# Kernel optimization log

Hardware: AMD Instinct MI355X
Metric: run time of the kernel (lower is better)

Reference implementation:

```python
import jax, jax.numpy as jnp
import numpy as np

B, S, D, H = 64, 128, 1024, 512
N = 2 * S - 1          # total tree nodes (leaves + internal)
NSTEP = S - 1          # number of binary compositions
NW, NP = 511, 152      # word / phrase category counts


def _l2n(x):
    return x / jnp.clip(jnp.linalg.norm(x, axis=-1, keepdims=True), 1e-12)


def circular_correlation(a, b):
    a, b = _l2n(a), _l2n(b)
    c = jnp.fft.irfft(jnp.conj(jnp.fft.rfft(a)) * jnp.fft.rfft(b), n=H)
    return _l2n(c)


def _lstm_dir(x, w_ih, w_hh, b):
    # x: [B,S,D] -> hs: [B,S,H]; PyTorch gate order i,f,g,o
    xp = jnp.einsum('bsd,gd->bsg', x, w_ih) + b  # precompute input proj

    def step(carry, xt):
        h, c = carry
        g = xt + h @ w_hh.T
        i, f, gg, o = jnp.split(g, 4, axis=-1)
        c = jax.nn.sigmoid(f) * c + jax.nn.sigmoid(i) * jnp.tanh(gg)
        h = jax.nn.sigmoid(o) * jnp.tanh(c)
        return (h, c), h

    h0 = jnp.zeros((x.shape[0], H), x.dtype)
    _, hs = jax.lax.scan(step, (h0, h0), xp.transpose(1, 0, 2))
    return hs.transpose(1, 0, 2)


def setup_inputs():
    key = jax.random.key(0)
    ks = jax.random.split(key, 12)
    sc = 0.05
    elmo_rep = jax.random.normal(ks[0], (B, S, D), jnp.float32)
    w_ih_f = jax.random.normal(ks[1], (4 * H, D), jnp.float32) * sc
    w_hh_f = jax.random.normal(ks[2], (4 * H, H), jnp.float32) * sc
    b_f = jnp.zeros((4 * H,), jnp.float32)
    w_ih_b = jax.random.normal(ks[3], (4 * H, D), jnp.float32) * sc
    w_hh_b = jax.random.normal(ks[4], (4 * H, H), jnp.float32) * sc
    b_b = jnp.zeros((4 * H,), jnp.float32)
    W1 = jax.random.normal(ks[5], (H, H), jnp.float32) * sc
    W2 = jax.random.normal(ks[6], (H, H), jnp.float32) * sc
    word_W = jax.random.normal(ks[7], (NW, H), jnp.float32) * sc
    word_b = jnp.zeros((NW,), jnp.float32)
    phrase_W = jax.random.normal(ks[8], (NP, H), jnp.float32) * sc
    phrase_b = jnp.zeros((NP,), jnp.float32)
    # valid binary-tree composition schedule: parent S+i, children < S+i
    rng = np.random.default_rng(0)
    comp = np.zeros((B, NSTEP, 4), np.int32)
    comp[:, :, 0] = 2
    for i in range(NSTEP):
        comp[:, i, 1] = S + i
        comp[:, i, 2] = rng.integers(0, S + i, size=B)
        comp[:, i, 3] = rng.integers(0, S + i, size=B)
    composition_info = jnp.asarray(comp)
    pos = jnp.stack([jnp.arange(S), jnp.arange(S)], axis=1).astype(jnp.int32)
    original_pos = jnp.tile(pos[None], (B, 1, 1))
    batch_label = jax.random.randint(ks[9], (B, N), 0, NW, dtype=jnp.int64)
    return dict(elmo_rep=elmo_rep, w_ih_f=w_ih_f, w_hh_f=w_hh_f, b_f=b_f,
                w_ih_b=w_ih_b, w_hh_b=w_hh_b, b_b=b_b, W1=W1, W2=W2,
                word_W=word_W, word_b=word_b, phrase_W=phrase_W,
                phrase_b=phrase_b, composition_info=composition_info,
                original_pos=original_pos, batch_label=batch_label)


def reference(elmo_rep, w_ih_f, w_hh_f, b_f, w_ih_b, w_hh_b, b_b, W1, W2,
              word_W, word_b, phrase_W, phrase_b, composition_info,
              original_pos, batch_label):
    # BiLSTM over ELMo reps (all sequences full length S)
    fwd = _lstm_dir(elmo_rep, w_ih_f, w_hh_f, b_f)
    bwd = _lstm_dir(elmo_rep[:, ::-1], w_ih_b, w_hh_b, b_b)[:, ::-1]
    combined = jax.nn.leaky_relu(fwd @ W1.T + bwd @ W2.T, negative_slope=0.01)

    # scatter leaves into node buffer [B,N,H], then L2-normalize
    bidx = jnp.arange(B)[:, None]
    tgt = original_pos[:, :, 0]
    src = original_pos[:, :, 1]
    vector = jnp.zeros((B, N, H), combined.dtype)
    vector = vector.at[bidx, tgt].set(combined[bidx, src])
    vector = _l2n(vector)

    # sequential per-depth compose: gather children, circular-correlate, scatter parent
    b = jnp.arange(B)

    def step(vec, info):  # info: [B,4] = [type, parent, left, right]
        t, p, l, r = info[:, 0], info[:, 1], info[:, 2], info[:, 3]
        lv = vec[b, l]
        rv = vec[b, r]
        comp = circular_correlation(lv, rv)
        cur = vec[b, p]
        val = jnp.where((t == 1)[:, None], lv,
                        jnp.where((t == 2)[:, None], comp, cur))
        return vec.at[b, p].set(val), None

    vector, _ = jax.lax.scan(step, vector, composition_info.transpose(1, 0, 2))

    # words = leaf nodes (first S slots), phrases = internal nodes
    word_vector = vector[:, :S].reshape(-1, H)
    phrase_vector = vector[:, S:].reshape(-1, H)
    word_label = batch_label[:, :S].reshape(-1)
    phrase_label = batch_label[:, S:].reshape(-1)
    word_output = word_vector @ word_W.T + word_b
    phrase_output = phrase_vector @ phrase_W.T + phrase_b
    return word_output, phrase_output, word_label, phrase_label
```

## Files before the change

kernel.cpp:

```cpp
#include <hip/hip_runtime.h>
#include <math.h>

#define NB 64
#define NS 128
#define ND 1024
#define NH 512
#define NG 2048
#define NTOT 255
#define NSTEPS 127
#define NWV 511
#define NPV 152

static const size_t XPB_SZ = (size_t)2 * NS * NG * NB;
static const size_t H_SZ   = (size_t)2 * NS * NH * NB;
static const size_t VEC_SZ = (size_t)NB * NTOT * NH;
static const size_t HB_SZ  = (size_t)2 * NS * NH * NB;
static const size_t EB_SZ  = (size_t)NB * NS * ND;
static const size_t WB_SZ  = (size_t)4096 * ND;
static const size_t W12_SZ = (size_t)2 * NH * NH;
static const size_t WO_SZ  = (size_t)512 * NH;
static const size_t VB_SZ  = (size_t)NB * NS * NH;
static const size_t VP_SZ  = (size_t)8192 * NH;
static const size_t WP_SZ  = (size_t)256 * NH;
#define BAR_TOT (127 * 2 * 32 * 32)

typedef __attribute__((ext_vector_type(8))) short short8v;
typedef __attribute__((ext_vector_type(8))) unsigned short ushort8v;
typedef __attribute__((ext_vector_type(4))) float float4v;

__device__ __forceinline__ float sigm(float x) { return 1.f / (1.f + __expf(-x)); }
__device__ __forceinline__ float tanh_fast(float x) {
  const float e = __expf(2.f * x);
  return 1.f - 2.f / (e + 1.f);
}
__device__ __forceinline__ unsigned short f2bf(float x) {
  unsigned b = __float_as_uint(x);
  return (unsigned short)((b + 0x7FFFu + ((b >> 16) & 1u)) >> 16);
}
__device__ __forceinline__ float bf2f(unsigned short u) {
  return __uint_as_float(((unsigned)u) << 16);
}

__global__ __launch_bounds__(256) void k_cvt(
    const float* __restrict__ elmo, const float* __restrict__ wf,
    const float* __restrict__ wb, const float* __restrict__ W1,
    const float* __restrict__ W2, const float* __restrict__ wordW,
    const float* __restrict__ phraseW,
    unsigned short* __restrict__ elmo_bf, unsigned short* __restrict__ W_bf,
    unsigned short* __restrict__ W12_bf, unsigned short* __restrict__ wout_bf,
    unsigned short* __restrict__ wp_bf, int* __restrict__ bar) {
  const int gid = blockIdx.x * 256 + threadIdx.x;
  if (gid < BAR_TOT) bar[gid] = 0;
  const int NE4 = (NB * NS * ND) / 4;
  const int NW4 = (4096 * ND) / 4;
  const int NW4h = NW4 / 2;
  const int N12 = (int)(W12_SZ / 4);
  const int NWO = (int)(WO_SZ / 4);
  const int NWO_real = (NWV * NH) / 4;
  const int NP4 = (int)(WP_SZ / 4);
  const int NP4_real = (NPV * NH) / 4;
  const int TOT = NE4 + NW4 + N12 + NWO + NP4;
  for (int i = gid; i < TOT; i += gridDim.x * 256) {
    float4 v = make_float4(0.f, 0.f, 0.f, 0.f);
    unsigned short* dst;
    if (i < NE4) {
      const int e0 = i << 2;
      const int b = e0 >> 17;
      const int t = (e0 >> 10) & 127;
      const int k = e0 & 1023;
      v = *(const float4*)(elmo + e0);
      dst = elmo_bf + ((size_t)((t << 6) + b) << 10) + k;
    } else if (i < NE4 + NW4) {
      const int j = i - NE4;
      v = (j < NW4h) ? *(const float4*)(wf + ((size_t)j << 2))
                     : *(const float4*)(wb + ((size_t)(j - NW4h) << 2));
      dst = W_bf + ((size_t)j << 2);
    } else if (i < NE4 + NW4 + N12) {
      const int j = i - NE4 - NW4;
      const int half = N12 / 2;
      v = (j < half) ? *(const float4*)(W1 + ((size_t)j << 2))
                     : *(const float4*)(W2 + ((size_t)(j - half) << 2));
      dst = W12_bf + ((size_t)j << 2);
    } else if (i < NE4 + NW4 + N12 + NWO) {
      const int j = i - NE4 - NW4 - N12;
      if (j < NWO_real) v = *(const float4*)(wordW + ((size_t)j << 2));
      dst = wout_bf + ((size_t)j << 2);
    } else {
      const int j = i - NE4 - NW4 - N12 - NWO;
      if (j < NP4_real) v = *(const float4*)(phraseW + ((size_t)j << 2));
      dst = wp_bf + ((size_t)j << 2);
    }
    uint2 u;
    u.x = (unsigned)f2bf(v.x) | ((unsigned)f2bf(v.y) << 16);
    u.y = (unsigned)f2bf(v.z) | ((unsigned)f2bf(v.w) << 16);
    *(uint2*)dst = u;
  }
}

__global__ __launch_bounds__(256) void k_xp(
    const unsigned short* __restrict__ elmo_bf,
    const unsigned short* __restrict__ W_bf,
    const float* __restrict__ biasf, const float* __restrict__ biasb,
    unsigned short* __restrict__ xpb) {
  __shared__ unsigned short As[128 * 64];
  __shared__ unsigned short Bs[128 * 64];
  const int tid = threadIdx.x;
  const int n0 = blockIdx.x * 128;
  const int m0 = blockIdx.y * 128;
  const int wv = tid >> 6, lane = tid & 63;
  const int cl = lane & 15, bq = lane >> 4;
  const int wm = (wv >> 1) << 6;
  const int wn = (wv & 1) << 6;
  const int sr = tid >> 1, skc = (tid & 1) << 5;
  const unsigned short* asrc = elmo_bf + (size_t)(m0 + sr) * ND + skc;
  const unsigned short* bsrc = W_bf + (size_t)(n0 + sr) * ND + skc;
  const int sswz = (sr & 15) << 3;
  float4v acc[4][4];
#pragma unroll
  for (int nt = 0; nt < 4; ++nt) {
    const int n = n0 + wn + nt * 16 + cl;
    const float bv = (n < 2048) ? biasf[n] : biasb[n - 2048];
#pragma unroll
    for (int mt = 0; mt < 4; ++mt) acc[mt][nt] = (float4v){bv, bv, bv, bv};
  }
  for (int k0 = 0; k0 < ND; k0 += 64) {
    ushort8v av4[4], bv4[4];
#pragma unroll
    for (int i = 0; i < 4; ++i) av4[i] = *(const ushort8v*)(asrc + k0 + 8 * i);
#pragma unroll
    for (int i = 0; i < 4; ++i) bv4[i] = *(const ushort8v*)(bsrc + k0 + 8 * i);
    __syncthreads();
#pragma unroll
    for (int i = 0; i < 4; ++i) {
      *(ushort8v*)&As[((sr << 6) + skc + 8 * i) ^ sswz] = av4[i];
      *(ushort8v*)&Bs[((sr << 6) + skc + 8 * i) ^ sswz] = bv4[i];
    }
    __syncthreads();
#pragma unroll
    for (int ks = 0; ks < 2; ++ks) {
      const int koff = (ks << 5) + (bq << 3);
      short8v af[4], bf_[4];
#pragma unroll
      for (int mt = 0; mt < 4; ++mt) {
        const int ar = wm + mt * 16 + cl;
        af[mt] = *(const short8v*)&As[((ar << 6) + koff) ^ ((ar & 15) << 3)];
      }
#pragma unroll
      for (int nt = 0; nt < 4; ++nt) {
        const int br = wn + nt * 16 + cl;
        bf_[nt] = *(const short8v*)&Bs[((br << 6) + koff) ^ ((br & 15) << 3)];
      }
#pragma unroll
      for (int mt = 0; mt < 4; ++mt)
#pragma unroll
        for (int nt = 0; nt < 4; ++nt)
          acc[mt][nt] =
              __builtin_amdgcn_mfma_f32_16x16x32_bf16(af[mt], bf_[nt], acc[mt][nt], 0, 0, 0);
    }
  }
#pragma unroll
  for (int mt = 0; mt < 4; ++mt) {
    const int mbase = m0 + wm + mt * 16 + (bq << 2);
    const int t = mbase >> 6, b4 = mbase & 63;
#pragma unroll
    for (int nt = 0; nt < 4; ++nt) {
      const int n = n0 + wn + nt * 16 + cl;
      const int dir = n >> 11, grow = n & 2047;
      const int g = grow >> 9, cb = (grow & 511) >> 4;
      const float4v a = acc[mt][nt];
      uint2 u;
      u.x = (unsigned)f2bf(a[0]) | ((unsigned)f2bf(a[1]) << 16);
      u.y = (unsigned)f2bf(a[2]) | ((unsigned)f2bf(a[3]) << 16);
      const size_t idx =
          ((((size_t)(dir * NS + t) * 32 + cb) * 4 + g) << 10) + (cl << 6) + b4;
      *(uint2*)&xpb[idx] = u;
    }
  }
}

__global__ __launch_bounds__(256) void k_lstm(
    const float* __restrict__ whh_f, const float* __restrict__ whh_b,
    const unsigned short* __restrict__ xpb,
    unsigned short* __restrict__ h_bf, int* __restrict__ bar) {
  __shared__ unsigned short WS[64 * 512];
  __shared__ unsigned short hOut[64 * 16];
  const int bid = blockIdx.x;
  const int dir = bid >> 5;
  const int cb = bid & 31;
  const int col0 = cb << 4;
  const int tid = threadIdx.x;
  const int lane = tid & 63;
  const int w = tid >> 6;
  const int cl = lane & 15, bq = lane >> 4;
  const int b4 = (w << 4) + (bq << 2);
  const int arow = (w << 4) + cl;
  const float* whh = dir ? whh_b : whh_f;

  {
    const int gr = tid >> 2;
    const int kc = (tid & 3) << 7;
    const int gg = gr >> 4, cc = gr & 15;
    const float* src = whh + (size_t)(gg * NH + col0 + cc) * NH + kc;
    const int swz = (gr & 15) << 3;
#pragma unroll
    for (int i = 0; i < 16; ++i) {
      const float4 f0 = *(const float4*)(src + 8 * i);
      const float4 f1 = *(const float4*)(src + 8 * i + 4);
      ushort8v u;
      u[0] = f2bf(f0.x); u[1] = f2bf(f0.y); u[2] = f2bf(f0.z); u[3] = f2bf(f0.w);
      u[4] = f2bf(f1.x); u[5] = f2bf(f1.y); u[6] = f2bf(f1.z); u[7] = f2bf(f1.w);
      *(ushort8v*)&WS[((gr << 9) + kc + 8 * i) ^ swz] = u;
    }
  }
  __syncthreads();

  unsigned short* hb_us = h_bf + ((size_t)dir * NS << 15);
  unsigned long long* hb_ull = (unsigned long long*)h_bf + ((size_t)dir * NS << 12);

  float4v c4 = {0.f, 0.f, 0.f, 0.f};

  uint2 xg0, xg1, xg2, xg3, xn0, xn1, xn2, xn3;
  {
    const int p0 = dir ? (NS - 1) : 0;
    const unsigned short* xc = xpb + (((size_t)(dir * NS + p0) * 32 + cb) << 12);
    xg0 = *(const uint2*)&xc[(0 << 10) + (cl << 6) + b4];
    xg1 = *(const uint2*)&xc[(1 << 10) + (cl << 6) + b4];
    xg2 = *(const uint2*)&xc[(2 << 10) + (cl << 6) + b4];
    xg3 = *(const uint2*)&xc[(3 << 10) + (cl << 6) + b4];
    const int p1 = dir ? (NS - 2) : 1;
    const unsigned short* xc1 = xpb + (((size_t)(dir * NS + p1) * 32 + cb) << 12);
    xn0 = *(const uint2*)&xc1[(0 << 10) + (cl << 6) + b4];
    xn1 = *(const uint2*)&xc1[(1 << 10) + (cl << 6) + b4];
    xn2 = *(const uint2*)&xc1[(2 << 10) + (cl << 6) + b4];
    xn3 = *(const uint2*)&xc1[(3 << 10) + (cl << 6) + b4];
  }

  for (int t = 0; t < NS; ++t) {
    const int pos = dir ? (NS - 1 - t) : t;
    const int t2 = (t + 2 < NS) ? (t + 2) : (NS - 1);
    const int p2 = dir ? (NS - 1 - t2) : t2;
    const unsigned short* xc2 =
        xpb + (((size_t)(dir * NS + p2) * 32 + cb) << 12);
    const uint2 pf0 = *(const uint2*)&xc2[(0 << 10) + (cl << 6) + b4];
    const uint2 pf1 = *(const uint2*)&xc2[(1 << 10) + (cl << 6) + b4];
    const uint2 pf2 = *(const uint2*)&xc2[(2 << 10) + (cl << 6) + b4];
    const uint2 pf3 = *(const uint2*)&xc2[(3 << 10) + (cl << 6) + b4];

    float4v acc[4] = {{0.f, 0.f, 0.f, 0.f}, {0.f, 0.f, 0.f, 0.f},
                      {0.f, 0.f, 0.f, 0.f}, {0.f, 0.f, 0.f, 0.f}};
    if (t > 0) {
      const int prevpos = dir ? (pos + 1) : (pos - 1);
      const unsigned long long* hsrc = hb_ull + ((size_t)prevpos << 13);
      unsigned long long ha0[16], ha1[16];
#pragma unroll
      for (int ks = 0; ks < 16; ++ks) {
        const int uidx = (arow << 7) + (ks << 3) + (bq << 1);
        ha0[ks] = __hip_atomic_load(&hsrc[uidx], __ATOMIC_RELAXED,
                                    __HIP_MEMORY_SCOPE_AGENT);
        ha1[ks] = __hip_atomic_load(&hsrc[uidx + 1], __ATOMIC_RELAXED,
                                    __HIP_MEMORY_SCOPE_AGENT);
      }
#pragma unroll
      for (int ks = 0; ks < 16; ++ks) {
        union { unsigned long long u[2]; short8v v; } au;
        au.u[0] = ha0[ks]; au.u[1] = ha1[ks];
        const short8v a = au.v;
        const int koff = (ks << 5) + (bq << 3);
#pragma unroll
        for (int g = 0; g < 4; ++g) {
          const short8v bb =
              *(const short8v*)&WS[((((g << 4) + cl) << 9) + koff) ^ (cl << 3)];
          acc[g] = __builtin_amdgcn_mfma_f32_16x16x32_bf16(a, bb, acc[g], 0, 0, 0);
        }
      }
    }
    float hv[4];
#pragma unroll
    for (int i = 0; i < 4; ++i) {
      const unsigned xw0 = (i < 2) ? xg0.x : xg0.y;
      const unsigned xw1 = (i < 2) ? xg1.x : xg1.y;
      const unsigned xw2 = (i < 2) ? xg2.x : xg2.y;
      const unsigned xw3 = (i < 2) ? xg3.x : xg3.y;
      const int sh = (i & 1) << 4;
      const float gi = sigm(acc[0][i] + bf2f((unsigned short)(xw0 >> sh)));
      const float gf = sigm(acc[1][i] + bf2f((unsigned short)(xw1 >> sh)));
      const float gc = tanh_fast(acc[2][i] + bf2f((unsigned short)(xw2 >> sh)));
      const float go = sigm(acc[3][i] + bf2f((unsigned short)(xw3 >> sh)));
      c4[i] = gf * c4[i] + gi * gc;
      hv[i] = go * tanh_fast(c4[i]);
    }
#pragma unroll
    for (int i = 0; i < 4; ++i) hOut[((b4 + i) << 4) + cl] = f2bf(hv[i]);
    __syncthreads();
    {
      const int bb = tid >> 2, q = tid & 3;
      const unsigned long long v =
          *(const unsigned long long*)&hOut[(bb << 4) + (q << 2)];
      __hip_atomic_store(
          (unsigned long long*)&hb_us[((size_t)pos << 15) + (bb << 9) + col0 +
                                      (q << 2)],
          v, __ATOMIC_RELAXED, __HIP_MEMORY_SCOPE_AGENT);
    }
    if (t < NS - 1) {
      __syncthreads();
      const int fbase = (((t << 1) + dir) << 5);
      if (tid == 0) {
        __hip_atomic_store(&bar[(size_t)(fbase + cb) << 5], 1,
                           __ATOMIC_RELAXED, __HIP_MEMORY_SCOPE_AGENT);
      }
      if (tid < 64) {
        const size_t fl = (size_t)(fbase + (lane & 31)) << 5;
        while (true) {
          int v = 1;
          if (lane < 32)
            v = __hip_atomic_load(&bar[fl], __ATOMIC_RELAXED,
                                  __HIP_MEMORY_SCOPE_AGENT);
          if (__all(v != 0)) break;
        }
      }
      __syncthreads();
      xg0 = xn0; xg1 = xn1; xg2 = xn2; xg3 = xn3;
      xn0 = pf0; xn1 = pf1; xn2 = pf2; xn3 = pf3;
    }
  }
}

__global__ __launch_bounds__(256) void k_comb(
    const unsigned short* __restrict__ h_bf,
    const unsigned short* __restrict__ W12_bf, float* __restrict__ vec) {
  __shared__ unsigned short A1s[64 * 128], A2s[64 * 128];
  __shared__ unsigned short B1s[64 * 128], B2s[64 * 128];
  const int tid = threadIdx.x;
  const int n0 = blockIdx.x * 64;
  const int s = blockIdx.y;
  const int w = tid >> 6, lane = tid & 63;
  const int cl = lane & 15, bq = lane >> 4;
  const int wn = w << 4;
  const unsigned short* a1src = h_bf + ((size_t)s << 15);
  const unsigned short* a2src = h_bf + ((size_t)(NS + s) << 15);
  const unsigned short* b1src = W12_bf + (size_t)n0 * NH;
  const unsigned short* b2src = W12_bf + (size_t)(NH + n0) * NH;
  const int srow = tid >> 2, skq = (tid & 3) << 5;
  const int sswz = (srow & 15) << 3;
  float4v acc[4] = {{0.f, 0.f, 0.f, 0.f}, {0.f, 0.f, 0.f, 0.f},
                    {0.f, 0.f, 0.f, 0.f}, {0.f, 0.f, 0.f, 0.f}};
  for (int k0 = 0; k0 < NH; k0 += 128) {
    ushort8v a1[4], a2[4], b1[4], b2[4];
#pragma unroll
    for (int i = 0; i < 4; ++i) {
      const size_t off = (size_t)srow * NH + k0 + skq + 8 * i;
      a1[i] = *(const ushort8v*)(a1src + off);
      a2[i] = *(const ushort8v*)(a2src + off);
      b1[i] = *(const ushort8v*)(b1src + off);
      b2[i] = *(const ushort8v*)(b2src + off);
    }
    __syncthreads();
#pragma unroll
    for (int i = 0; i < 4; ++i) {
      const int idx = ((srow << 7) + skq + 8 * i) ^ sswz;
      *(ushort8v*)&A1s[idx] = a1[i];
      *(ushort8v*)&A2s[idx] = a2[i];
      *(ushort8v*)&B1s[idx] = b1[i];
      *(ushort8v*)&B2s[idx] = b2[i];
    }
    __syncthreads();
#pragma unroll
    for (int ks = 0; ks < 4; ++ks) {
      const int koff = (ks << 5) + (bq << 3);
      const short8v bf1 =
          *(const short8v*)&B1s[(((wn + cl) << 7) + koff) ^ (cl << 3)];
      const short8v bf2 =
          *(const short8v*)&B2s[(((wn + cl) << 7) + koff) ^ (cl << 3)];
#pragma unroll
      for (int mt = 0; mt < 4; ++mt) {
        const int ar = mt * 16 + cl;
        const short8v af1 = *(const short8v*)&A1s[((ar << 7) + koff) ^ (cl << 3)];
        const short8v af2 = *(const short8v*)&A2s[((ar << 7) + koff) ^ (cl << 3)];
        acc[mt] = __builtin_amdgcn_mfma_f32_16x16x32_bf16(af1, bf1, acc[mt], 0, 0, 0);
        acc[mt] = __builtin_amdgcn_mfma_f32_16x16x32_bf16(af2, bf2, acc[mt], 0, 0, 0);
      }
    }
  }
  const int n = n0 + wn + cl;
#pragma unroll
  for (int mt = 0; mt < 4; ++mt) {
    const int b0 = mt * 16 + (bq << 2);
#pragma unroll
    for (int i = 0; i < 4; ++i) {
      float v = acc[mt][i];
      v = v > 0.f ? v : 0.01f * v;
      vec[((size_t)(b0 + i) * NTOT + s) * NH + n] = v;
    }
  }
}

__global__ __launch_bounds__(256) void k_norm(float* __restrict__ vec,
                                              unsigned short* __restrict__ vec_bf) {
  const int row = (blockIdx.x << 2) + (threadIdx.x >> 6);
  const int lane = threadIdx.x & 63;
  const int b = row >> 7, s = row & 127;
  float* p = vec + ((size_t)b * NTOT + s) * NH;
  float4 v0 = *(float4*)(p + (lane << 3));
  float4 v1 = *(float4*)(p + (lane << 3) + 4);
  float ss = v0.x * v0.x + v0.y * v0.y + v0.z * v0.z + v0.w * v0.w +
             v1.x * v1.x + v1.y * v1.y + v1.z * v1.z + v1.w * v1.w;
#pragma unroll
  for (int off = 32; off; off >>= 1) ss += __shfl_down(ss, off);
  ss = __shfl(ss, 0);
  const float sc = 1.f / fmaxf(sqrtf(ss), 1e-12f);
  v0.x *= sc; v0.y *= sc; v0.z *= sc; v0.w *= sc;
  v1.x *= sc; v1.y *= sc; v1.z *= sc; v1.w *= sc;
  *(float4*)(p + (lane << 3)) = v0;
  *(float4*)(p + (lane << 3) + 4) = v1;
  ushort8v u;
  u[0] = f2bf(v0.x); u[1] = f2bf(v0.y); u[2] = f2bf(v0.z); u[3] = f2bf(v0.w);
  u[4] = f2bf(v1.x); u[5] = f2bf(v1.y); u[6] = f2bf(v1.z); u[7] = f2bf(v1.w);
  *(ushort8v*)&vec_bf[((size_t)row << 9) + (lane << 3)] = u;
}

#define SKW(f) ((f) + (((f) >> 5) << 2))
__global__ __launch_bounds__(512) void k_tail(
    float* __restrict__ vec, const int* __restrict__ cinfo,
    unsigned short* __restrict__ vecp_bf,
    const unsigned short* __restrict__ vec_bf,
    const unsigned short* __restrict__ wout_bf,
    const float* __restrict__ wbias, float* __restrict__ out_word,
    const int* __restrict__ lab, float* __restrict__ out_lw,
    float* __restrict__ out_lp) {
  __shared__ float lv[512];
  __shared__ float rvd[1152];
  __shared__ float cpart[8 * 576];
  __shared__ float red[8];
  __shared__ int ciS[NSTEPS * 4];
  __shared__ unsigned short As[128 * 64];
  __shared__ unsigned short Bs[128 * 64];
  const int bid = blockIdx.x;
  const int tid = threadIdx.x;

  if (bid < 64) {
    const int b = bid;
    float* vb = vec + (size_t)b * NTOT * NH;
    const int* ib = cinfo + b * NSTEPS * 4;
    for (int idx = tid; idx < NSTEPS * 4; idx += 512) ciS[idx] = ib[idx];
    const int jq = tid >> 6;
    const int jb = jq << 6;
    const int k8 = (tid & 63) << 3;
    const int wid = tid >> 6, lane = tid & 63;
    __syncthreads();
    int p = ciS[1];
    float lvv = vb[(size_t)ciS[2] * NH + tid];
    float rvv = vb[(size_t)ciS[3] * NH + tid];
    for (int i = 0; i < NSTEPS; ++i) {
      lv[tid] = lvv;
      rvd[SKW(tid)] = rvv;
      rvd[SKW(512 + tid)] = rvv;
      __syncthreads();
      float acc[8] = {};
#pragma unroll 4
      for (int jj = 0; jj < 64; jj += 4) {
        const int j = jb + jj;
        const float4 l4 = *(const float4*)&lv[j];
        const int f0 = j + k8;
        const float4 r0 = *(const float4*)&rvd[SKW(f0)];
        const float4 r1 = *(const float4*)&rvd[SKW(f0 + 4)];
        const float4 r2 = *(const float4*)&rvd[SKW(f0 + 8)];
        const float rw[12] = {r0.x, r0.y, r0.z, r0.w, r1.x, r1.y,
                              r1.z, r1.w, r2.x, r2.y, r2.z, r2.w};
#pragma unroll
        for (int kk = 0; kk < 8; ++kk)
          acc[kk] += l4.x * rw[kk] + l4.y * rw[kk + 1] + l4.z * rw[kk + 2] +
                     l4.w * rw[kk + 3];
      }
      const int ca = jq * 576 + SKW(k8);
      *(float4*)&cpart[ca] = make_float4(acc[0], acc[1], acc[2], acc[3]);
      *(float4*)&cpart[ca + 4] = make_float4(acc[4], acc[5], acc[6], acc[7]);
      __syncthreads();
      int pn = 0, ln = 0, rn = 0;
      float lf = 0.f, rf = 0.f;
      const bool more = (i + 1 < NSTEPS);
      if (more) {
        pn = ciS[(i + 1) * 4 + 1];
        ln = ciS[(i + 1) * 4 + 2];
        rn = ciS[(i + 1) * 4 + 3];
        lf = vb[(size_t)ln * NH + tid];
        rf = vb[(size_t)rn * NH + tid];
      }
      float ck = 0.f;
      const int ra = SKW(tid);
#pragma unroll
      for (int q = 0; q < 8; ++q) ck += cpart[q * 576 + ra];
      float ss = ck * ck;
#pragma unroll
      for (int off = 32; off; off >>= 1) ss += __shfl_xor(ss, off);
      if (lane == 0) red[wid] = ss;
      __syncthreads();
      const float tot = red[0] + red[1] + red[2] + red[3] +
                        red[4] + red[5] + red[6] + red[7];
      const float inv = 1.f / fmaxf(sqrtf(tot), 1e-12f);
      const float written = ck * inv;
      vb[(size_t)p * NH + tid] = written;
      vecp_bf[((size_t)b * 127 + (p - NS)) * NH + tid] = f2bf(written);
      if (more) {
        lvv = (ln == p) ? written : lf;
        rvv = (rn == p) ? written : rf;
        p = pn;
      }
      __syncthreads();
    }
  } else if (bid < 320) {
    const int obid = bid - 64;
    const int n0 = (obid & 3) * 128;
    const int m0 = (obid >> 2) * 128;
    const int wv = tid >> 6, lane = tid & 63;
    const int cl = lane & 15, bq = lane >> 4;
    const int wm = (wv >> 2) << 6;
    const int wn = ((wv >> 1) & 1) << 6;
    const int mts = (wv & 1) << 1;
    const int sr = tid >> 2, skc = (tid & 3) << 4;
    const unsigned short* asrc = vec_bf + (size_t)(m0 + sr) * NH + skc;
    const unsigned short* bsrc = wout_bf + (size_t)(n0 + sr) * NH + skc;
    const int sswz = (sr & 15) << 3;
    float4v acc[2][4] = {};
    for (int k0 = 0; k0 < NH; k0 += 64) {
      ushort8v av4[2], bv4[2];
#pragma unroll
      for (int i = 0; i < 2; ++i) av4[i] = *(const ushort8v*)(asrc + k0 + 8 * i);
#pragma unroll
      for (int i = 0; i < 2; ++i) bv4[i] = *(const ushort8v*)(bsrc + k0 + 8 * i);
      __syncthreads();
#pragma unroll
      for (int i = 0; i < 2; ++i) {
        *(ushort8v*)&As[((sr << 6) + skc + 8 * i) ^ sswz] = av4[i];
        *(ushort8v*)&Bs[((sr << 6) + skc + 8 * i) ^ sswz] = bv4[i];
      }
      __syncthreads();
#pragma unroll
      for (int ks = 0; ks < 2; ++ks) {
        const int koff = (ks << 5) + (bq << 3);
        short8v af[2], bf_[4];
#pragma unroll
        for (int mtl = 0; mtl < 2; ++mtl) {
          const int ar = wm + (mts + mtl) * 16 + cl;
          af[mtl] = *(const short8v*)&As[((ar << 6) + koff) ^ ((ar & 15) << 3)];
        }
#pragma unroll
        for (int nt = 0; nt < 4; ++nt) {
          const int br = wn + nt * 16 + cl;
          bf_[nt] = *(const short8v*)&Bs[((br << 6) + koff) ^ ((br & 15) << 3)];
        }
#pragma unroll
        for (int mtl = 0; mtl < 2; ++mtl)
#pragma unroll
          for (int nt = 0; nt < 4; ++nt)
            acc[mtl][nt] = __builtin_amdgcn_mfma_f32_16x16x32_bf16(
                af[mtl], bf_[nt], acc[mtl][nt], 0, 0, 0);
      }
    }
#pragma unroll
    for (int mtl = 0; mtl < 2; ++mtl) {
      const int mb = m0 + wm + (mts + mtl) * 16 + (bq << 2);
#pragma unroll
      for (int nt = 0; nt < 4; ++nt) {
        const int n = n0 + wn + nt * 16 + cl;
        if (n < NWV) {
          const float bn = wbias[n];
#pragma unroll
          for (int i = 0; i < 4; ++i)
            out_word[(size_t)(mb + i) * NWV + n] = acc[mtl][nt][i] + bn;
        }
      }
    }
  } else {
    const int i = (bid - 320) * 512 + tid;
    if (i < NB * NS) {
      const int b = i >> 7, s = i & 127;
      out_lw[i] = (float)lab[b * NTOT + s];
    }
    if (i < NB * NSTEPS) {
      const int b = i / 127;
      out_lp[i] = (float)lab[b * NTOT + NS + (i - b * 127)];
    }
  }
}

__global__ __launch_bounds__(256) void k_outp(
    const unsigned short* __restrict__ vecp_bf,
    const unsigned short* __restrict__ wp_bf,
    const float* __restrict__ bias, float* __restrict__ out) {
  __shared__ unsigned short As[128 * 64];
  __shared__ unsigned short Bs[128 * 64];
  const int tid = threadIdx.x;
  const int n0 = blockIdx.x * 128;
  const int m0 = blockIdx.y * 128;
  const int wv = tid >> 6, lane = tid & 63;
  const int cl = lane & 15, bq = lane >> 4;
  const int wm = (wv >> 1) << 6;
  const int wn = (wv & 1) << 6;
  const int sr = tid >> 1, skc = (tid & 1) << 5;
  const unsigned short* asrc = vecp_bf + (size_t)(m0 + sr) * NH + skc;
  const unsigned short* bsrc = wp_bf + (size_t)(n0 + sr) * NH + skc;
  const int sswz = (sr & 15) << 3;
  float4v acc[4][4] = {};
  for (int k0 = 0; k0 < NH; k0 += 64) {
    ushort8v av4[4], bv4[4];
#pragma unroll
    for (int i = 0; i < 4; ++i) av4[i] = *(const ushort8v*)(asrc + k0 + 8 * i);
#pragma unroll
    for (int i = 0; i < 4; ++i) bv4[i] = *(const ushort8v*)(bsrc + k0 + 8 * i);
    __syncthreads();
#pragma unroll
    for (int i = 0; i < 4; ++i) {
      *(ushort8v*)&As[((sr << 6) + skc + 8 * i) ^ sswz] = av4[i];
      *(ushort8v*)&Bs[((sr << 6) + skc + 8 * i) ^ sswz] = bv4[i];
    }
    __syncthreads();
#pragma unroll
    for (int ks = 0; ks < 2; ++ks) {
      const int koff = (ks << 5) + (bq << 3);
      short8v af[4], bf_[4];
#pragma unroll
      for (int mt = 0; mt < 4; ++mt) {
        const int ar = wm + mt * 16 + cl;
        af[mt] = *(const short8v*)&As[((ar << 6) + koff) ^ ((ar & 15) << 3)];
      }
#pragma unroll
      for (int nt = 0; nt < 4; ++nt) {
        const int br = wn + nt * 16 + cl;
        bf_[nt] = *(const short8v*)&Bs[((br << 6) + koff) ^ ((br & 15) << 3)];
      }
#pragma unroll
      for (int mt = 0; mt < 4; ++mt)
#pragma unroll
        for (int nt = 0; nt < 4; ++nt)
          acc[mt][nt] =
              __builtin_amdgcn_mfma_f32_16x16x32_bf16(af[mt], bf_[nt], acc[mt][nt], 0, 0, 0);
    }
  }
#pragma unroll
  for (int mt = 0; mt < 4; ++mt) {
    const int mb = m0 + wm + mt * 16 + (bq << 2);
#pragma unroll
    for (int nt = 0; nt < 4; ++nt) {
      const int n = n0 + wn + nt * 16 + cl;
      if (n < NPV) {
        const float bn = bias[n];
#pragma unroll
        for (int i = 0; i < 4; ++i)
          if (mb + i < 8128)
            out[(size_t)(mb + i) * NPV + n] = acc[mt][nt][i] + bn;
      }
    }
  }
}

extern "C" void kernel_launch(void* const* d_in, const int* in_sizes, int n_in,
                              void* d_out, int out_size, void* d_ws, size_t ws_size,
                              hipStream_t stream) {
  (void)in_sizes; (void)n_in; (void)out_size; (void)ws_size;
  const float* elmo     = (const float*)d_in[0];
  const float* w_ih_f   = (const float*)d_in[1];
  const float* w_hh_f   = (const float*)d_in[2];
  const float* b_f      = (const float*)d_in[3];
  const float* w_ih_b   = (const float*)d_in[4];
  const float* w_hh_b   = (const float*)d_in[5];
  const float* b_b      = (const float*)d_in[6];
  const float* W1       = (const float*)d_in[7];
  const float* W2       = (const float*)d_in[8];
  const float* word_W   = (const float*)d_in[9];
  const float* word_b   = (const float*)d_in[10];
  const float* phrase_W = (const float*)d_in[11];
  const float* phrase_b = (const float*)d_in[12];
  const int* cinfo      = (const int*)d_in[13];
  const int* lab        = (const int*)d_in[15];

  unsigned short* xpb   = (unsigned short*)d_ws;
  float* h_region       = (float*)(xpb + XPB_SZ);
  unsigned short* vecp_bf = (unsigned short*)h_region;
  unsigned short* wp_bf   = vecp_bf + VP_SZ;
  float* vec            = h_region + H_SZ;
  unsigned short* h_bf  = (unsigned short*)(vec + VEC_SZ);
  unsigned short* e_bf  = h_bf + HB_SZ;
  unsigned short* W_bf  = e_bf + EB_SZ;
  unsigned short* W12_bf  = W_bf + WB_SZ;
  unsigned short* wout_bf = W12_bf + W12_SZ;
  unsigned short* vec_bf  = wout_bf + WO_SZ;
  int* bar              = (int*)(vec_bf + VB_SZ);

  float* out_word = (float*)d_out;
  float* out_phr  = out_word + (size_t)8192 * NWV;
  float* out_lw   = out_phr + (size_t)8128 * NPV;
  float* out_lp   = out_lw + 8192;

  k_cvt<<<dim3(2048), 256, 0, stream>>>(elmo, w_ih_f, w_ih_b, W1, W2, word_W,
                                        phrase_W, e_bf, W_bf, W12_bf, wout_bf,
                                        wp_bf, bar);
  k_xp<<<dim3(32, 64), 256, 0, stream>>>(e_bf, W_bf, b_f, b_b, xpb);
  k_lstm<<<dim3(64), 256, 0, stream>>>(w_hh_f, w_hh_b, xpb, h_bf, bar);
  k_comb<<<dim3(8, 128), 256, 0, stream>>>(h_bf, W12_bf, vec);
  k_norm<<<dim3(2048), 256, 0, stream>>>(vec, vec_bf);
  k_tail<<<dim3(336), 512, 0, stream>>>(vec, cinfo, vecp_bf, vec_bf, wout_bf,
                                        word_b, out_word, lab, out_lw, out_lp);
  k_outp<<<dim3(2, 64), 256, 0, stream>>>(vecp_bf, wp_bf, phrase_b, out_phr);
}
```

Before: 1.518 ms.

## Halve LSTM blocks to 32 columns each and reuse correlation register window

The persistent LSTM recurrence kernel now runs 32 blocks, each owning 32 hidden columns (128 gate rows of W_hh in LDS), instead of 64 blocks owning 16. Each step does twice the MFMA work per block, but the per-step grid barrier only has to poll 16 flags, which is meant to reduce synchronisation latency on the sequential critical path. The two-step-ahead register prefetch of the input projection is dropped in favour of loading it directly each step. Separately, the circular-correlation inner loop now carries the rvd float4 window in registers across iterations, so each iteration loads one vector from LDS instead of three.

```diff
diff --git a/kernel.cpp b/kernel.cpp
--- a/kernel.cpp
+++ b/kernel.cpp
@@ -182,12 +182,12 @@
     const float* __restrict__ whh_f, const float* __restrict__ whh_b,
     const unsigned short* __restrict__ xpb,
     unsigned short* __restrict__ h_bf, int* __restrict__ bar) {
-  __shared__ unsigned short WS[64 * 512];
-  __shared__ unsigned short hOut[64 * 16];
+  __shared__ unsigned short WS[128 * 512];
+  __shared__ __align__(16) unsigned short hOut[64 * 32];
   const int bid = blockIdx.x;
-  const int dir = bid >> 5;
-  const int cb = bid & 31;
-  const int col0 = cb << 4;
+  const int dir = bid >> 4;
+  const int cb = bid & 15;
+  const int col0 = cb << 5;
   const int tid = threadIdx.x;
   const int lane = tid & 63;
   const int w = tid >> 6;
@@ -197,19 +197,19 @@
   const float* whh = dir ? whh_b : whh_f;
 
   {
-    const int gr = tid >> 2;
-    const int kc = (tid & 3) << 7;
-    const int gg = gr >> 4, cc = gr & 15;
-    const float* src = whh + (size_t)(gg * NH + col0 + cc) * NH + kc;
+    const int gr = tid >> 1;
+    const int kh = (tid & 1) << 8;
+    const int g = gr >> 5, c = gr & 31;
+    const float* src = whh + (size_t)(g * NH + col0 + c) * NH + kh;
     const int swz = (gr & 15) << 3;
 #pragma unroll
-    for (int i = 0; i < 16; ++i) {
+    for (int i = 0; i < 32; ++i) {
       const float4 f0 = *(const float4*)(src + 8 * i);
       const float4 f1 = *(const float4*)(src + 8 * i + 4);
       ushort8v u;
       u[0] = f2bf(f0.x); u[1] = f2bf(f0.y); u[2] = f2bf(f0.z); u[3] = f2bf(f0.w);
       u[4] = f2bf(f1.x); u[5] = f2bf(f1.y); u[6] = f2bf(f1.z); u[7] = f2bf(f1.w);
-      *(ushort8v*)&WS[((gr << 9) + kc + 8 * i) ^ swz] = u;
+      *(ushort8v*)&WS[((gr << 9) + kh + 8 * i) ^ swz] = u;
     }
   }
   __syncthreads();
@@ -217,37 +217,23 @@
   unsigned short* hb_us = h_bf + ((size_t)dir * NS << 15);
   unsigned long long* hb_ull = (unsigned long long*)h_bf + ((size_t)dir * NS << 12);
 
-  float4v c4 = {0.f, 0.f, 0.f, 0.f};
-
-  uint2 xg0, xg1, xg2, xg3, xn0, xn1, xn2, xn3;
-  {
-    const int p0 = dir ? (NS - 1) : 0;
-    const unsigned short* xc = xpb + (((size_t)(dir * NS + p0) * 32 + cb) << 12);
-    xg0 = *(const uint2*)&xc[(0 << 10) + (cl << 6) + b4];
-    xg1 = *(const uint2*)&xc[(1 << 10) + (cl << 6) + b4];
-    xg2 = *(const uint2*)&xc[(2 << 10) + (cl << 6) + b4];
-    xg3 = *(const uint2*)&xc[(3 << 10) + (cl << 6) + b4];
-    const int p1 = dir ? (NS - 2) : 1;
-    const unsigned short* xc1 = xpb + (((size_t)(dir * NS + p1) * 32 + cb) << 12);
-    xn0 = *(const uint2*)&xc1[(0 << 10) + (cl << 6) + b4];
-    xn1 = *(const uint2*)&xc1[(1 << 10) + (cl << 6) + b4];
-    xn2 = *(const uint2*)&xc1[(2 << 10) + (cl << 6) + b4];
-    xn3 = *(const uint2*)&xc1[(3 << 10) + (cl << 6) + b4];
-  }
+  float4v c4lo = {0.f, 0.f, 0.f, 0.f};
+  float4v c4hi = {0.f, 0.f, 0.f, 0.f};
 
   for (int t = 0; t < NS; ++t) {
     const int pos = dir ? (NS - 1 - t) : t;
-    const int t2 = (t + 2 < NS) ? (t + 2) : (NS - 1);
-    const int p2 = dir ? (NS - 1 - t2) : t2;
-    const unsigned short* xc2 =
-        xpb + (((size_t)(dir * NS + p2) * 32 + cb) << 12);
-    const uint2 pf0 = *(const uint2*)&xc2[(0 << 10) + (cl << 6) + b4];
-    const uint2 pf1 = *(const uint2*)&xc2[(1 << 10) + (cl << 6) + b4];
-    const uint2 pf2 = *(const uint2*)&xc2[(2 << 10) + (cl << 6) + b4];
-    const uint2 pf3 = *(const uint2*)&xc2[(3 << 10) + (cl << 6) + b4];
-
-    float4v acc[4] = {{0.f, 0.f, 0.f, 0.f}, {0.f, 0.f, 0.f, 0.f},
-                      {0.f, 0.f, 0.f, 0.f}, {0.f, 0.f, 0.f, 0.f}};
+    const unsigned short* xcl =
+        xpb + (((size_t)(dir * NS + pos) * 32 + (cb << 1)) << 12);
+    const unsigned short* xch = xcl + 4096;
+    uint2 xlo[4], xhi[4];
+#pragma unroll
+    for (int g = 0; g < 4; ++g) {
+      xlo[g] = *(const uint2*)&xcl[(g << 10) + (cl << 6) + b4];
+      xhi[g] = *(const uint2*)&xch[(g << 10) + (cl << 6) + b4];
+    }
+    float4v acc[8] = {{0.f,0.f,0.f,0.f},{0.f,0.f,0.f,0.f},{0.f,0.f,0.f,0.f},
+                      {0.f,0.f,0.f,0.f},{0.f,0.f,0.f,0.f},{0.f,0.f,0.f,0.f},
+                      {0.f,0.f,0.f,0.f},{0.f,0.f,0.f,0.f}};
     if (t > 0) {
       const int prevpos = dir ? (pos + 1) : (pos - 1);
       const unsigned long long* hsrc = hb_ull + ((size_t)prevpos << 13);
@@ -267,60 +253,71 @@
         const short8v a = au.v;
         const int koff = (ks << 5) + (bq << 3);
 #pragma unroll
-        for (int g = 0; g < 4; ++g) {
+        for (int nt = 0; nt < 8; ++nt) {
+          const int grb = (nt << 4) + cl;
           const short8v bb =
-              *(const short8v*)&WS[((((g << 4) + cl) << 9) + koff) ^ (cl << 3)];
-          acc[g] = __builtin_amdgcn_mfma_f32_16x16x32_bf16(a, bb, acc[g], 0, 0, 0);
+              *(const short8v*)&WS[((grb << 9) + koff) ^ (cl << 3)];
+          acc[nt] = __builtin_amdgcn_mfma_f32_16x16x32_bf16(a, bb, acc[nt], 0, 0, 0);
         }
       }
     }
-    float hv[4];
 #pragma unroll
     for (int i = 0; i < 4; ++i) {
-      const unsigned xw0 = (i < 2) ? xg0.x : xg0.y;
-      const unsigned xw1 = (i < 2) ? xg1.x : xg1.y;
-      const unsigned xw2 = (i < 2) ? xg2.x : xg2.y;
-      const unsigned xw3 = (i < 2) ? xg3.x : xg3.y;
       const int sh = (i & 1) << 4;
-      const float gi = sigm(acc[0][i] + bf2f((unsigned short)(xw0 >> sh)));
-      const float gf = sigm(acc[1][i] + bf2f((unsigned short)(xw1 >> sh)));
-      const float gc = tanh_fast(acc[2][i] + bf2f((unsigned short)(xw2 >> sh)));
-      const float go = sigm(acc[3][i] + bf2f((unsigned short)(xw3 >> sh)));
-      c4[i] = gf * c4[i] + gi * gc;
-      hv[i] = go * tanh_fast(c4[i]);
-    }
-#pragma unroll
-    for (int i = 0; i < 4; ++i) hOut[((b4 + i) << 4) + cl] = f2bf(hv[i]);
+      {
+        const unsigned x0 = (i < 2) ? xlo[0].x : xlo[0].y;
+        const unsigned x1 = (i < 2) ? xlo[1].x : xlo[1].y;
+        const unsigned x2 = (i < 2) ? xlo[2].x : xlo[2].y;
+        const unsigned x3 = (i < 2) ? xlo[3].x : xlo[3].y;
+        const float gi = sigm(acc[0][i] + bf2f((unsigned short)(x0 >> sh)));
+        const float gf = sigm(acc[2][i] + bf2f((unsigned short)(x1 >> sh)));
+        const float gc = tanh_fast(acc[4][i] + bf2f((unsigned short)(x2 >> sh)));
+        const float go = sigm(acc[6][i] + bf2f((unsigned short)(x3 >> sh)));
+        c4lo[i] = gf * c4lo[i] + gi * gc;
+        hOut[((b4 + i) << 5) + cl] = f2bf(go * tanh_fast(c4lo[i]));
+      }
+      {
+        const unsigned x0 = (i < 2) ? xhi[0].x : xhi[0].y;
+        const unsigned x1 = (i < 2) ? xhi[1].x : xhi[1].y;
+        const unsigned x2 = (i < 2) ? xhi[2].x : xhi[2].y;
+        const unsigned x3 = (i < 2) ? xhi[3].x : xhi[3].y;
+        const float gi = sigm(acc[1][i] + bf2f((unsigned short)(x0 >> sh)));
+        const float gf = sigm(acc[3][i] + bf2f((unsigned short)(x1 >> sh)));
+        const float gc = tanh_fast(acc[5][i] + bf2f((unsigned short)(x2 >> sh)));
+        const float go = sigm(acc[7][i] + bf2f((unsigned short)(x3 >> sh)));
+        c4hi[i] = gf * c4hi[i] + gi * gc;
+        hOut[((b4 + i) << 5) + cl + 16] = f2bf(go * tanh_fast(c4hi[i]));
+      }
+    }
     __syncthreads();
     {
       const int bb = tid >> 2, q = tid & 3;
-      const unsigned long long v =
-          *(const unsigned long long*)&hOut[(bb << 4) + (q << 2)];
-      __hip_atomic_store(
-          (unsigned long long*)&hb_us[((size_t)pos << 15) + (bb << 9) + col0 +
-                                      (q << 2)],
-          v, __ATOMIC_RELAXED, __HIP_MEMORY_SCOPE_AGENT);
+      const unsigned long long* src =
+          (const unsigned long long*)&hOut[(bb << 5) + (q << 3)];
+      const unsigned long long v0 = src[0];
+      const unsigned long long v1 = src[1];
+      unsigned long long* dst = (unsigned long long*)&hb_us[
+          ((size_t)pos << 15) + (bb << 9) + col0 + (q << 3)];
+      __hip_atomic_store(&dst[0], v0, __ATOMIC_RELAXED, __HIP_MEMORY_SCOPE_AGENT);
+      __hip_atomic_store(&dst[1], v1, __ATOMIC_RELAXED, __HIP_MEMORY_SCOPE_AGENT);
     }
     if (t < NS - 1) {
       __syncthreads();
-      const int fbase = (((t << 1) + dir) << 5);
+      const int fbase = (((t << 1) + dir) << 4);
       if (tid == 0) {
         __hip_atomic_store(&bar[(size_t)(fbase + cb) << 5], 1,
                            __ATOMIC_RELAXED, __HIP_MEMORY_SCOPE_AGENT);
       }
       if (tid < 64) {
-        const size_t fl = (size_t)(fbase + (lane & 31)) << 5;
         while (true) {
           int v = 1;
-          if (lane < 32)
-            v = __hip_atomic_load(&bar[fl], __ATOMIC_RELAXED,
-                                  __HIP_MEMORY_SCOPE_AGENT);
+          if (lane < 16)
+            v = __hip_atomic_load(&bar[(size_t)(fbase + lane) << 5],
+                                  __ATOMIC_RELAXED, __HIP_MEMORY_SCOPE_AGENT);
           if (__all(v != 0)) break;
         }
       }
       __syncthreads();
-      xg0 = xn0; xg1 = xn1; xg2 = xn2; xg3 = xn3;
-      xn0 = pf0; xn1 = pf1; xn2 = pf2; xn3 = pf3;
     }
   }
 }
@@ -456,20 +453,20 @@
       rvd[SKW(512 + tid)] = rvv;
       __syncthreads();
       float acc[8] = {};
+      float4 r0 = *(const float4*)&rvd[SKW(jb + k8)];
+      float4 r1 = *(const float4*)&rvd[SKW(jb + k8 + 4)];
 #pragma unroll 4
       for (int jj = 0; jj < 64; jj += 4) {
         const int j = jb + jj;
         const float4 l4 = *(const float4*)&lv[j];
-        const int f0 = j + k8;
-        const float4 r0 = *(const float4*)&rvd[SKW(f0)];
-        const float4 r1 = *(const float4*)&rvd[SKW(f0 + 4)];
-        const float4 r2 = *(const float4*)&rvd[SKW(f0 + 8)];
+        const float4 r2 = *(const float4*)&rvd[SKW(j + k8 + 8)];
         const float rw[12] = {r0.x, r0.y, r0.z, r0.w, r1.x, r1.y,
                               r1.z, r1.w, r2.x, r2.y, r2.z, r2.w};
 #pragma unroll
         for (int kk = 0; kk < 8; ++kk)
           acc[kk] += l4.x * rw[kk] + l4.y * rw[kk + 1] + l4.z * rw[kk + 2] +
                      l4.w * rw[kk + 3];
+        r0 = r1; r1 = r2;
       }
       const int ca = jq * 576 + SKW(k8);
       *(float4*)&cpart[ca] = make_float4(acc[0], acc[1], acc[2], acc[3]);
@@ -695,7 +692,7 @@
                                         phrase_W, e_bf, W_bf, W12_bf, wout_bf,
                                         wp_bf, bar);
   k_xp<<<dim3(32, 64), 256, 0, stream>>>(e_bf, W_bf, b_f, b_b, xpb);
-  k_lstm<<<dim3(64), 256, 0, stream>>>(w_hh_f, w_hh_b, xpb, h_bf, bar);
+  k_lstm<<<dim3(32), 256, 0, stream>>>(w_hh_f, w_hh_b, xpb, h_bf, bar);
   k_comb<<<dim3(8, 128), 256, 0, stream>>>(h_bf, W12_bf, vec);
   k_norm<<<dim3(2048), 256, 0, stream>>>(vec, vec_bf);
   k_tail<<<dim3(336), 512, 0, stream>>>(vec, cinfo, vecp_bf, vec_bf, wout_bf,
```

New measurement: 1.735 ms. +14.3%, slower.
